# Kernel tuning notes

Measured on AMD Instinct MI355X. Metric: run time of the kernel, lower is better.

The kernel has to match this reference:

```python
import jax, jax.numpy as jnp
import numpy as np


def setup_inputs() -> dict:
    key = jax.random.key(0)
    k1, k2 = jax.random.split(key)
    f = jax.random.normal(k1, (4, 8192, 3), dtype=jnp.float32)
    f_ = jax.random.normal(k2, (4, 8192, 3), dtype=jnp.float32)
    return {"f": f, "f_": f_}


def _square_distance(src, dst):
    # src: [B,N,3], dst: [B,M,3] -> [B,N,M]
    # ||s-d||^2 = ||s||^2 + ||d||^2 - 2 s.d
    cross = jnp.einsum("bnc,bmc->bnm", src, dst)  # [B,N,M]
    s2 = jnp.sum(src * src, axis=-1)[:, :, None]   # [B,N,1]
    d2 = jnp.sum(dst * dst, axis=-1)[:, None, :]   # [B,1,M]
    return s2 + d2 - 2.0 * cross


def reference(f, f_):
    dis = _square_distance(f, f_)
    dis = jnp.maximum(dis, 0.0)  # dis[dis <= 0] = 0
    f2f_ = jnp.min(dis, axis=2)  # [B,N] nearest in f_ for each point of f
    f_2f = jnp.min(dis, axis=1)  # [B,M] nearest in f for each point of f_
    d = jnp.mean(f2f_, axis=1) + jnp.mean(f_2f, axis=1)  # [B]
    return jnp.mean(d)
```

## Files before the change

kernel.cpp:

```cpp
#include <hip/hip_runtime.h>

#define NPTS  8192
#define BATCH 4
#define RN    4
#define BWAVES 8

typedef float v2f __attribute__((ext_vector_type(2)));


__global__ void pack_kernel(const float* __restrict__ f,
                            const float* __restrict__ f_,
                            float4* __restrict__ pk,
                            float*  __restrict__ prf,
                            float*  __restrict__ out) {
    int j = blockIdx.x * blockDim.x + threadIdx.x;
    if (j == 0) out[0] = 0.0f;
    const float* src = (j >= 32768) ? f_ : f;
    int idx = j & 32767;
    float x = src[idx * 3 + 0];
    float y = src[idx * 3 + 1];
    float z = src[idx * 3 + 2];
    float w = -0.5f * (x * x + y * y + z * z);
    pk[j] = make_float4(x, y, z, w);
    int  slot = j & 1;
    long base = (long)(j >> 1) * 8;
    prf[base + 0 + slot] = x;
    prf[base + 2 + slot] = y;
    prf[base + 4 + slot] = z;
    prf[base + 6 + slot] = w;
}

__global__ __launch_bounds__(512, 8) void chamfer_main(
        const float4* __restrict__ pk, const float4* __restrict__ pr,
        float* __restrict__ seg) {
    __shared__ float red[BWAVES][256];

    int tid  = threadIdx.x;
    int wv   = __builtin_amdgcn_readfirstlane(tid >> 6);
    int lane = tid & 63;

    int bx   = blockIdx.x;
    int tile = bx & 31;
    int b    = (bx >> 5) & 3;
    int dir  = (bx >> 7) & 1;
    int mq   = bx >> 8;

    const float4* __restrict__ A = pk + ((size_t)dir * BATCH + b) * NPTS;
    int n_base = tile * 256;
    v2f px[RN], py[RN], pz[RN], e2[RN];
#pragma unroll
    for (int r = 0; r < RN; ++r) {
        float4 p = A[n_base + lane + 64 * r];
        px[r] = (v2f){p.x, p.x};
        py[r] = (v2f){p.y, p.y};
        pz[r] = (v2f){p.z, p.z};
        e2[r] = (v2f){-1e30f, -1e30f};
    }

    int sb_m = (1 - dir) * BATCH + b;
    const float4* __restrict__ mp =
        pr + ((size_t)sb_m * 4096 + mq * 1024 + wv * 128) * 2;

    for (int i = 0; i < 128; i += 4) {
#pragma unroll
        for (int u = 0; u < 4; ++u) {
            float4 qa = mp[(i + u) * 2 + 0];
            float4 qb = mp[(i + u) * 2 + 1];
            v2f qx = (v2f){qa.x, qa.y};
            v2f qy = (v2f){qa.z, qa.w};
            v2f qz = (v2f){qb.x, qb.y};
            v2f qw = (v2f){qb.z, qb.w};
#pragma unroll
            for (int r = 0; r < RN; ++r) {
                v2f c = __builtin_elementwise_fma(px[r], qx, qw);
                c = __builtin_elementwise_fma(py[r], qy, c);
                c = __builtin_elementwise_fma(pz[r], qz, c);
                e2[r] = __builtin_elementwise_max(e2[r], c);
            }
        }
    }

#pragma unroll
    for (int r = 0; r < RN; ++r)
        red[wv][lane + 64 * r] = fmaxf(e2[r].x, e2[r].y);
    __syncthreads();

    if (tid < 256) {
        float emax = red[0][tid];
#pragma unroll
        for (int ww = 1; ww < BWAVES; ++ww) emax = fmaxf(emax, red[ww][tid]);
        seg[mq * (2 * BATCH * NPTS) + dir * (BATCH * NPTS) + b * NPTS
            + n_base + tid] = emax;
    }
}

__global__ __launch_bounds__(1024) void chamfer_finalize(
        const float4* __restrict__ pk, const float* __restrict__ seg,
        float* __restrict__ out) {
    __shared__ float partial[16];
    int j = blockIdx.x * 1024 + threadIdx.x;
    float emax = seg[j];
#pragma unroll
    for (int q = 1; q < 4; ++q) emax = fmaxf(emax, seg[q * 65536 + j]);
    float dist = fmaxf(-2.0f * (emax + pk[j].w), 0.0f);
    for (int off = 32; off > 0; off >>= 1)
        dist += __shfl_down(dist, off, 64);
    int lane = threadIdx.x & 63, wv = threadIdx.x >> 6;
    if (lane == 0) partial[wv] = dist;
    __syncthreads();
    if (threadIdx.x < 16) {
        float s = partial[threadIdx.x];
        for (int off = 8; off > 0; off >>= 1)
            s += __shfl_down(s, off, 64);
        if (threadIdx.x == 0) atomicAdd(out, s * (1.0f / 32768.0f));
    }
}


__global__ void zero_out_kernel(float* __restrict__ out) { out[0] = 0.0f; }

__global__ __launch_bounds__(1024) void chamfer_fallback(
        const float* __restrict__ f, const float* __restrict__ f_,
        float* __restrict__ out) {
    __shared__ float wlds[NPTS];
    __shared__ float red[16][256];
    __shared__ float partial[4];

    int tid  = threadIdx.x;
    int wv   = __builtin_amdgcn_readfirstlane(tid >> 6);
    int lane = tid & 63;

    int bx   = blockIdx.x;
    int dir  = bx >> 7;
    int b    = (bx >> 5) & 3;
    int tile = bx & 31;
    int n_base = tile * 256;

    const float* __restrict__ A  = dir ? f_ : f;
    const float* __restrict__ Bm = dir ? f  : f_;
    const float* an = A  + (size_t)b * NPTS * 3;
    const float* bm = Bm + (size_t)b * NPTS * 3;

    for (int i = tid; i < NPTS; i += 1024) {
        float x = bm[i * 3 + 0], y = bm[i * 3 + 1], z = bm[i * 3 + 2];
        wlds[i] = -0.5f * (x * x + y * y + z * z);
    }

    float xn[RN], yn[RN], zn[RN];
#pragma unroll
    for (int r = 0; r < RN; ++r) {
        int n = n_base + lane + 64 * r;
        xn[r] = an[n * 3 + 0];
        yn[r] = an[n * 3 + 1];
        zn[r] = an[n * 3 + 2];
    }
    __syncthreads();

    float e[RN];
#pragma unroll
    for (int r = 0; r < RN; ++r) e[r] = -1e30f;

    int m0 = wv * (NPTS / 16);
#pragma unroll 4
    for (int i = 0; i < NPTS / 16; ++i) {
        int m = m0 + i;
        float qx = bm[m * 3 + 0], qy = bm[m * 3 + 1], qz = bm[m * 3 + 2];
        float qw = wlds[m];
#pragma unroll
        for (int r = 0; r < RN; ++r) {
            float c = fmaf(zn[r], qz, fmaf(yn[r], qy, fmaf(xn[r], qx, qw)));
            e[r] = fmaxf(e[r], c);
        }
    }

#pragma unroll
    for (int r = 0; r < RN; ++r) red[wv][lane + 64 * r] = e[r];
    __syncthreads();

    if (tid < 256) {
        float emax = red[0][tid];
#pragma unroll
        for (int ww = 1; ww < 16; ++ww) emax = fmaxf(emax, red[ww][tid]);
        int n = n_base + tid;
        float x = an[n * 3 + 0], y = an[n * 3 + 1], z = an[n * 3 + 2];
        float dist = fmaxf(x * x + y * y + z * z - 2.0f * emax, 0.0f);
        for (int off = 32; off > 0; off >>= 1)
            dist += __shfl_down(dist, off, 64);
        if ((tid & 63) == 0) partial[tid >> 6] = dist;
    }
    __syncthreads();
    if (tid == 0) {
        float s = partial[0] + partial[1] + partial[2] + partial[3];
        atomicAdd(out, s * (1.0f / 32768.0f));
    }
}

extern "C" void kernel_launch(void* const* d_in, const int* in_sizes, int n_in,
                              void* d_out, int out_size, void* d_ws, size_t ws_size,
                              hipStream_t stream) {
    const float* f  = (const float*)d_in[0];
    const float* f_ = (const float*)d_in[1];
    float* out = (float*)d_out;

    const size_t PK_B  = 65536 * sizeof(float4);
    const size_t PR_B  = 65536 * sizeof(float4);
    const size_t SEG_B = 262144 * sizeof(float);
    if (ws_size >= PK_B + PR_B + SEG_B) {
        float4* pk = (float4*)d_ws;
        float4* pr = (float4*)((char*)d_ws + PK_B);
        float*  sg = (float*)((char*)d_ws + PK_B + PR_B);
        pack_kernel<<<256, 256, 0, stream>>>(f, f_, pk, (float*)pr, out);
        chamfer_main<<<1024, 512, 0, stream>>>(pk, pr, sg);
        chamfer_finalize<<<64, 1024, 0, stream>>>(pk, sg, out);
    } else {
        zero_out_kernel<<<1, 1, 0, stream>>>(out);
        chamfer_fallback<<<256, 1024, 0, stream>>>(f, f_, out);
    }
}
```

Measured before the change: 98.84 us.

## Compute chamfer distances with bf16 split-precision MFMA instead of FP32 FMA

Adds a new path that packs each point into hi/lo bf16 components, including the -0.5*|p|^2 term, so the augmented dot product reproduces s·d - |d|^2/2 - |s|^2/2 through a 16x16x32 bf16 MFMA. The per-pair distance is then a matrix-core output that is max-reduced per row and shuffled across lanes. It is meant to move the O(N*M) inner work from vector FMAs onto the matrix cores. Half the lanes feed zeros and the hi/lo split drops the lo*lo cross terms, so precision is lower. This path is used only when the workspace is at least 5 MB, which is more than before.

```diff
diff --git a/kernel.cpp b/kernel.cpp
--- a/kernel.cpp
+++ b/kernel.cpp
@@ -2,24 +2,159 @@
 
 #define NPTS  8192
 #define BATCH 4
-#define RN    4
-#define BWAVES 8
-
-typedef float v2f __attribute__((ext_vector_type(2)));
-
-
-__global__ void pack_kernel(const float* __restrict__ f,
-                            const float* __restrict__ f_,
-                            float4* __restrict__ pk,
-                            float*  __restrict__ prf,
-                            float*  __restrict__ out) {
+
+typedef short  bf8   __attribute__((ext_vector_type(8)));
+typedef float  f32x4 __attribute__((ext_vector_type(4)));
+typedef float  v2f   __attribute__((ext_vector_type(2)));
+
+__device__ inline unsigned short bf16_rne(float x) {
+    unsigned u = __float_as_uint(x);
+    unsigned r = (u + 0x7FFFu + ((u >> 16) & 1u)) >> 16;
+    return (unsigned short)r;
+}
+__device__ inline float bf16_to_f(unsigned short h) {
+    return __uint_as_float(((unsigned)h) << 16);
+}
+
+
+__global__ void pack_mfma(const float* __restrict__ f, const float* __restrict__ f_,
+                          bf8* __restrict__ fA, bf8* __restrict__ fB,
+                          bf8* __restrict__ gA, bf8* __restrict__ gB,
+                          float* __restrict__ out) {
+    int j = blockIdx.x * blockDim.x + threadIdx.x;
+    if (j == 0) out[0] = 0.0f;
+    int cloud = j >> 15;
+    int idx   = j & 32767;
+    const float* src = cloud ? f_ : f;
+    float x = src[idx * 3 + 0], y = src[idx * 3 + 1], z = src[idx * 3 + 2];
+    float w = -0.5f * (x * x + y * y + z * z);
+    unsigned short xh = bf16_rne(x), yh = bf16_rne(y), zh = bf16_rne(z);
+    unsigned short xl = bf16_rne(x - bf16_to_f(xh));
+    unsigned short yl = bf16_rne(y - bf16_to_f(yh));
+    unsigned short zl = bf16_rne(z - bf16_to_f(zh));
+    unsigned short wh = bf16_rne(w);
+    unsigned short wl = bf16_rne(w - bf16_to_f(wh));
+    const short ONE = (short)0x3F80;
+
+    bf8 A0, A1, B0, B1;
+    A0[0]=(short)xh; A0[1]=(short)yh; A0[2]=(short)zh; A0[3]=(short)xl;
+    A0[4]=(short)yl; A0[5]=(short)zl; A0[6]=(short)xh; A0[7]=(short)yh;
+    A1[0]=(short)zh; A1[1]=ONE;       A1[2]=ONE;       A1[3]=(short)wh;
+    A1[4]=(short)wl; A1[5]=0;         A1[6]=0;         A1[7]=0;
+    B0[0]=(short)xh; B0[1]=(short)yh; B0[2]=(short)zh; B0[3]=(short)xh;
+    B0[4]=(short)yh; B0[5]=(short)zh; B0[6]=(short)xl; B0[7]=(short)yl;
+    B1[0]=(short)zl; B1[1]=(short)wh; B1[2]=(short)wl; B1[3]=ONE;
+    B1[4]=ONE;       B1[5]=0;         B1[6]=0;         B1[7]=0;
+
+    int b = idx >> 13, p = idx & 8191;
+    int t = p >> 4, li = p & 15;
+    size_t slot = ((size_t)(b * 512 + t)) * 32;
+    bf8* Adst = cloud ? gA : fA;
+    bf8* Bdst = cloud ? gB : fB;
+    Adst[slot + li]      = A0;
+    Adst[slot + 16 + li] = A1;
+    Bdst[slot + li]      = B0;
+    Bdst[slot + 16 + li] = B1;
+}
+
+__global__ __launch_bounds__(256) void chamfer_mfma(
+        const bf8* __restrict__ fA, const bf8* __restrict__ fB,
+        const bf8* __restrict__ gA, const bf8* __restrict__ gB,
+        float* __restrict__ seg) {
+    int tid  = threadIdx.x;
+    int wv   = tid >> 6, lane = tid & 63;
+    int bx   = blockIdx.x;
+    int mseg = bx & 3;
+    int nblk = (bx >> 2) & 31;
+    int b    = (bx >> 7) & 3;
+    int pass = bx >> 9;
+
+    const bf8* __restrict__ Af = pass ? gA : fA;
+    const bf8* __restrict__ Bf = pass ? fB : gB;
+
+    bf8 zero = {};
+    bf8 a[4];
+    f32x4 rmax[4];
+    int nt_base = b * 512 + nblk * 16 + wv * 4;
+#pragma unroll
+    for (int s = 0; s < 4; ++s) {
+        a[s] = (lane < 32) ? Af[(size_t)(nt_base + s) * 32 + lane] : zero;
+        rmax[s] = (f32x4)(-3.0e38f);
+    }
+
+    const bf8* __restrict__ bp = Bf + ((size_t)(b * 512 + mseg * 128)) * 32;
+    bf8 bq = (lane < 32) ? bp[lane] : zero;
+    f32x4 zc = (f32x4)(0.0f);
+
+    for (int i = 0; i < 128; ++i) {
+        int ip = (i + 1 < 128) ? i + 1 : 127;
+        bf8 nx = (lane < 32) ? bp[(size_t)ip * 32 + lane] : zero;
+#pragma unroll
+        for (int s = 0; s < 4; ++s) {
+            f32x4 d = __builtin_amdgcn_mfma_f32_16x16x32_bf16(a[s], bq, zc, 0, 0, 0);
+            rmax[s] = __builtin_elementwise_max(rmax[s], d);
+        }
+        bq = nx;
+    }
+
+#pragma unroll
+    for (int s = 0; s < 4; ++s) {
+#pragma unroll
+        for (int m = 1; m < 16; m <<= 1) {
+            f32x4 o;
+            o[0] = __shfl_xor(rmax[s][0], m, 64);
+            o[1] = __shfl_xor(rmax[s][1], m, 64);
+            o[2] = __shfl_xor(rmax[s][2], m, 64);
+            o[3] = __shfl_xor(rmax[s][3], m, 64);
+            rmax[s] = __builtin_elementwise_max(rmax[s], o);
+        }
+    }
+
+    if ((lane & 15) == 0) {
+        int quad = lane >> 4;
+        float* sg = seg + ((size_t)((pass * 4 + b) * 4 + mseg)) * NPTS
+                        + nblk * 256 + wv * 64;
+#pragma unroll
+        for (int s = 0; s < 4; ++s)
+#pragma unroll
+            for (int r = 0; r < 4; ++r)
+                sg[s * 16 + quad * 4 + r] = rmax[s][r];
+    }
+}
+
+__global__ __launch_bounds__(1024) void finalize_mfma(
+        const float* __restrict__ seg, float* __restrict__ out) {
+    __shared__ float partial[16];
+    int j  = blockIdx.x * 1024 + threadIdx.x;
+    int pb = j >> 13;
+    int n  = j & 8191;
+    float emax = -3.0e38f;
+#pragma unroll
+    for (int q = 0; q < 4; ++q)
+        emax = fmaxf(emax, seg[((size_t)(pb * 4 + q)) * NPTS + n]);
+    float dist = fmaxf(-2.0f * emax, 0.0f);
+    for (int off = 32; off > 0; off >>= 1)
+        dist += __shfl_down(dist, off, 64);
+    int lane = threadIdx.x & 63, wv = threadIdx.x >> 6;
+    if (lane == 0) partial[wv] = dist;
+    __syncthreads();
+    if (threadIdx.x < 16) {
+        float s = partial[threadIdx.x];
+        for (int off = 8; off > 0; off >>= 1)
+            s += __shfl_down(s, off, 64);
+        if (threadIdx.x == 0) atomicAdd(out, s * (1.0f / 32768.0f));
+    }
+}
+
+
+__global__ void pack_pk(const float* __restrict__ f, const float* __restrict__ f_,
+                        float4* __restrict__ pk, float* __restrict__ prf,
+                        float* __restrict__ out) {
     int j = blockIdx.x * blockDim.x + threadIdx.x;
     if (j == 0) out[0] = 0.0f;
     const float* src = (j >= 32768) ? f_ : f;
     int idx = j & 32767;
-    float x = src[idx * 3 + 0];
-    float y = src[idx * 3 + 1];
-    float z = src[idx * 3 + 2];
+    float x = src[idx * 3 + 0], y = src[idx * 3 + 1], z = src[idx * 3 + 2];
     float w = -0.5f * (x * x + y * y + z * z);
     pk[j] = make_float4(x, y, z, w);
     int  slot = j & 1;
@@ -30,15 +165,13 @@
     prf[base + 6 + slot] = w;
 }
 
-__global__ __launch_bounds__(512, 8) void chamfer_main(
+__global__ __launch_bounds__(512, 8) void chamfer_pk(
         const float4* __restrict__ pk, const float4* __restrict__ pr,
         float* __restrict__ seg) {
-    __shared__ float red[BWAVES][256];
-
+    __shared__ float red[8][256];
     int tid  = threadIdx.x;
     int wv   = __builtin_amdgcn_readfirstlane(tid >> 6);
     int lane = tid & 63;
-
     int bx   = blockIdx.x;
     int tile = bx & 31;
     int b    = (bx >> 5) & 3;
@@ -47,16 +180,15 @@
 
     const float4* __restrict__ A = pk + ((size_t)dir * BATCH + b) * NPTS;
     int n_base = tile * 256;
-    v2f px[RN], py[RN], pz[RN], e2[RN];
-#pragma unroll
-    for (int r = 0; r < RN; ++r) {
+    v2f px[4], py[4], pz[4], e2[4];
+#pragma unroll
+    for (int r = 0; r < 4; ++r) {
         float4 p = A[n_base + lane + 64 * r];
         px[r] = (v2f){p.x, p.x};
         py[r] = (v2f){p.y, p.y};
         pz[r] = (v2f){p.z, p.z};
         e2[r] = (v2f){-1e30f, -1e30f};
     }
-
     int sb_m = (1 - dir) * BATCH + b;
     const float4* __restrict__ mp =
         pr + ((size_t)sb_m * 4096 + mq * 1024 + wv * 128) * 2;
@@ -71,7 +203,7 @@
             v2f qz = (v2f){qb.x, qb.y};
             v2f qw = (v2f){qb.z, qb.w};
 #pragma unroll
-            for (int r = 0; r < RN; ++r) {
+            for (int r = 0; r < 4; ++r) {
                 v2f c = __builtin_elementwise_fma(px[r], qx, qw);
                 c = __builtin_elementwise_fma(py[r], qy, c);
                 c = __builtin_elementwise_fma(pz[r], qz, c);
@@ -79,22 +211,20 @@
             }
         }
     }
-
-#pragma unroll
-    for (int r = 0; r < RN; ++r)
+#pragma unroll
+    for (int r = 0; r < 4; ++r)
         red[wv][lane + 64 * r] = fmaxf(e2[r].x, e2[r].y);
     __syncthreads();
-
     if (tid < 256) {
         float emax = red[0][tid];
 #pragma unroll
-        for (int ww = 1; ww < BWAVES; ++ww) emax = fmaxf(emax, red[ww][tid]);
+        for (int ww = 1; ww < 8; ++ww) emax = fmaxf(emax, red[ww][tid]);
         seg[mq * (2 * BATCH * NPTS) + dir * (BATCH * NPTS) + b * NPTS
             + n_base + tid] = emax;
     }
 }
 
-__global__ __launch_bounds__(1024) void chamfer_finalize(
+__global__ __launch_bounds__(1024) void finalize_pk(
         const float4* __restrict__ pk, const float* __restrict__ seg,
         float* __restrict__ out) {
     __shared__ float partial[16];
@@ -125,41 +255,32 @@
     __shared__ float wlds[NPTS];
     __shared__ float red[16][256];
     __shared__ float partial[4];
-
     int tid  = threadIdx.x;
     int wv   = __builtin_amdgcn_readfirstlane(tid >> 6);
     int lane = tid & 63;
-
     int bx   = blockIdx.x;
     int dir  = bx >> 7;
     int b    = (bx >> 5) & 3;
     int tile = bx & 31;
     int n_base = tile * 256;
-
     const float* __restrict__ A  = dir ? f_ : f;
     const float* __restrict__ Bm = dir ? f  : f_;
     const float* an = A  + (size_t)b * NPTS * 3;
     const float* bm = Bm + (size_t)b * NPTS * 3;
-
     for (int i = tid; i < NPTS; i += 1024) {
         float x = bm[i * 3 + 0], y = bm[i * 3 + 1], z = bm[i * 3 + 2];
         wlds[i] = -0.5f * (x * x + y * y + z * z);
     }
-
-    float xn[RN], yn[RN], zn[RN];
-#pragma unroll
-    for (int r = 0; r < RN; ++r) {
+    float xn[4], yn[4], zn[4];
+#pragma unroll
+    for (int r = 0; r < 4; ++r) {
         int n = n_base + lane + 64 * r;
-        xn[r] = an[n * 3 + 0];
-        yn[r] = an[n * 3 + 1];
-        zn[r] = an[n * 3 + 2];
-    }
-    __syncthreads();
-
-    float e[RN];
-#pragma unroll
-    for (int r = 0; r < RN; ++r) e[r] = -1e30f;
-
+        xn[r] = an[n * 3 + 0]; yn[r] = an[n * 3 + 1]; zn[r] = an[n * 3 + 2];
+    }
+    __syncthreads();
+    float e[4];
+#pragma unroll
+    for (int r = 0; r < 4; ++r) e[r] = -1e30f;
     int m0 = wv * (NPTS / 16);
 #pragma unroll 4
     for (int i = 0; i < NPTS / 16; ++i) {
@@ -167,16 +288,14 @@
         float qx = bm[m * 3 + 0], qy = bm[m * 3 + 1], qz = bm[m * 3 + 2];
         float qw = wlds[m];
 #pragma unroll
-        for (int r = 0; r < RN; ++r) {
+        for (int r = 0; r < 4; ++r) {
             float c = fmaf(zn[r], qz, fmaf(yn[r], qy, fmaf(xn[r], qx, qw)));
             e[r] = fmaxf(e[r], c);
         }
     }
-
-#pragma unroll
-    for (int r = 0; r < RN; ++r) red[wv][lane + 64 * r] = e[r];
-    __syncthreads();
-
+#pragma unroll
+    for (int r = 0; r < 4; ++r) red[wv][lane + 64 * r] = e[r];
+    __syncthreads();
     if (tid < 256) {
         float emax = red[0][tid];
 #pragma unroll
@@ -202,16 +321,23 @@
     const float* f_ = (const float*)d_in[1];
     float* out = (float*)d_out;
 
-    const size_t PK_B  = 65536 * sizeof(float4);
-    const size_t PR_B  = 65536 * sizeof(float4);
-    const size_t SEG_B = 262144 * sizeof(float);
-    if (ws_size >= PK_B + PR_B + SEG_B) {
+    const size_t MB = 1048576;
+    if (ws_size >= 5 * MB) {
+        bf8*   fA  = (bf8*)d_ws;
+        bf8*   fB  = (bf8*)((char*)d_ws + 1 * MB);
+        bf8*   gA  = (bf8*)((char*)d_ws + 2 * MB);
+        bf8*   gB  = (bf8*)((char*)d_ws + 3 * MB);
+        float* seg = (float*)((char*)d_ws + 4 * MB);
+        pack_mfma<<<256, 256, 0, stream>>>(f, f_, fA, fB, gA, gB, out);
+        chamfer_mfma<<<1024, 256, 0, stream>>>(fA, fB, gA, gB, seg);
+        finalize_mfma<<<64, 1024, 0, stream>>>(seg, out);
+    } else if (ws_size >= 3 * MB) {
         float4* pk = (float4*)d_ws;
-        float4* pr = (float4*)((char*)d_ws + PK_B);
-        float*  sg = (float*)((char*)d_ws + PK_B + PR_B);
-        pack_kernel<<<256, 256, 0, stream>>>(f, f_, pk, (float*)pr, out);
-        chamfer_main<<<1024, 512, 0, stream>>>(pk, pr, sg);
-        chamfer_finalize<<<64, 1024, 0, stream>>>(pk, sg, out);
+        float4* pr = (float4*)((char*)d_ws + 1 * MB);
+        float*  sg = (float*)((char*)d_ws + 2 * MB);
+        pack_pk<<<256, 256, 0, stream>>>(f, f_, pk, (float*)pr, out);
+        chamfer_pk<<<1024, 512, 0, stream>>>(pk, pr, sg);
+        finalize_pk<<<64, 1024, 0, stream>>>(pk, sg, out);
     } else {
         zero_out_kernel<<<1, 1, 0, stream>>>(out);
         chamfer_fallback<<<256, 1024, 0, stream>>>(f, f_, out);
```

New measurement: 142.1 us. 1.44x slower.
